# Performance work log

Hardware: AMD Instinct MI355X
Metric: run time of the kernel (lower is better)

## Reference

```python
import jax, jax.numpy as jnp
import numpy as np

# static 3D multi-scale configuration (transoar-style)
SS = np.array([[24, 24, 24], [12, 12, 12], [6, 6, 6], [3, 3, 3]], dtype=np.int64)  # (D,H,W) per level
NPL = SS.prod(1)
LSI = np.concatenate([[0], np.cumsum(NPL)[:-1]]).astype(np.int64)
S = int(NPL.sum())  # 15795 flattened tokens
B, C, HH, L, P = 2, 256, 8, 4, 4
DH = C // HH
NQ, FF = 80, 1024
NENC, NDEC = 6, 6
EPS = 1e-5


def layer_norm(x, g, b):
    mu = jnp.mean(x, -1, keepdims=True)
    var = jnp.mean((x - mu) ** 2, -1, keepdims=True)
    return (x - mu) * jax.lax.rsqrt(var + EPS) * g + b


def mha(q, k, v, in_w, in_b, out_w, out_b, mask=None):
    # torch nn.MultiheadAttention math (batch-first layout here)
    wq, wk, wv = jnp.split(in_w, 3, 0)
    bq, bk, bv = jnp.split(in_b, 3, 0)
    qh = (q @ wq.T + bq).reshape(B, -1, HH, DH)
    kh = (k @ wk.T + bk).reshape(B, -1, HH, DH)
    vh = (v @ wv.T + bv).reshape(B, -1, HH, DH)
    logits = jnp.einsum('bqhd,bkhd->bhqk', qh, kh) / jnp.float32(np.sqrt(DH))
    if mask is not None:  # bool mask, True = blocked
        logits = jnp.where(mask[None, None], jnp.float32(-1e9), logits)
    att = jax.nn.softmax(logits, -1)
    o = jnp.einsum('bhqk,bkhd->bqhd', att, vh).reshape(B, -1, C)
    return o @ out_w.T + out_b


def ms_deform_attn(query, ref, value_in, off_w, off_b, aw_w, aw_b, val_w, val_b, out_w, out_b):
    # 3D multi-scale deformable attention (deformable-DETR, trilinear sampling,
    # zero padding outside, align_corners=False semantics)
    Nq = query.shape[1]
    value = (value_in @ val_w.T + val_b).reshape(B, S, HH, DH)
    off = (query @ off_w.T + off_b).reshape(B, Nq, HH, L, P, 3)
    aw = jax.nn.softmax((query @ aw_w.T + aw_b).reshape(B, Nq, HH, L * P), -1)
    aw = aw.reshape(B, Nq, HH, L, P)
    norm = jnp.asarray(SS[:, ::-1].copy(), jnp.float32)  # (W,H,D) per level -> xyz order
    loc = ref[:, :, None, :, None, :] + off / norm[None, None, None, :, None, :]  # [B,Nq,HH,L,P,3]
    out = jnp.zeros((B, Nq, HH, DH), query.dtype)
    for lvl in range(L):
        D_, H_, W_ = (int(s) for s in SS[lvl])
        s0 = int(LSI[lvl])
        v = value[:, s0:s0 + D_ * H_ * W_].transpose(0, 2, 1, 3).reshape(B * HH, D_ * H_ * W_, DH)
        l = loc[:, :, :, lvl].transpose(0, 2, 1, 3, 4).reshape(B * HH, Nq * P, 3)
        x = l[..., 0] * W_ - 0.5
        y = l[..., 1] * H_ - 0.5
        z = l[..., 2] * D_ - 0.5
        x0, y0, z0 = jnp.floor(x), jnp.floor(y), jnp.floor(z)
        samp = jnp.zeros((B * HH, Nq * P, DH), query.dtype)
        for dz in (0, 1):
            for dy in (0, 1):
                for dx in (0, 1):
                    xi, yi, zi = x0 + dx, y0 + dy, z0 + dz
                    w = (1 - jnp.abs(x - xi)) * (1 - jnp.abs(y - yi)) * (1 - jnp.abs(z - zi))
                    ok = (xi >= 0) & (xi < W_) & (yi >= 0) & (yi < H_) & (zi >= 0) & (zi < D_)
                    idx = ((jnp.clip(zi, 0, D_ - 1) * H_ + jnp.clip(yi, 0, H_ - 1)) * W_
                           + jnp.clip(xi, 0, W_ - 1)).astype(jnp.int32)
                    samp = samp + jnp.take_along_axis(v, idx[..., None], axis=1) * (w * ok)[..., None]
        samp = samp.reshape(B, HH, Nq, P, DH)
        out = out + jnp.einsum('bhqpd,bhqp->bqhd', samp, aw[:, :, :, lvl].transpose(0, 2, 1, 3))
    return out.reshape(B, Nq, C) @ out_w.T + out_b


def get_reference_points(valid_ratios):
    refs = []
    for D_, H_, W_ in SS:
        z = (np.arange(D_) + 0.5) / D_
        y = (np.arange(H_) + 0.5) / H_
        x = (np.arange(W_) + 0.5) / W_
        zz, yy, xx = np.meshgrid(z, y, x, indexing='ij')
        refs.append(np.stack([xx.ravel(), yy.ravel(), zz.ravel()], -1))
    ref = jnp.asarray(np.concatenate(refs, 0).astype(np.float32))  # [S,3] xyz
    return ref[None, :, None, :] * valid_ratios[:, None]  # [B,S,L,3]


def _forward(fl, attn_mask):
    (src, pos, lvl_pos, tgt, query_pos, valid_ratios,
     eow, eob, eaw, eab, evw, evb, eouw, eoub, el1g, el1b, ef1w, ef1b, ef2w, ef2b, el2g, el2b,
     dsiw, dsib, dsow, dsob, dciw, dcib, dcow, dcob,
     dl1g, dl1b, dl2g, dl2b, dl3g, dl3b, df1w, df1b, df2w, df2b) = fl
    ref = get_reference_points(valid_ratios)
    out = src
    for i in range(NENC):
        a = ms_deform_attn(out + pos, ref, out, eow[i], eob[i], eaw[i], eab[i],
                           evw[i], evb[i], eouw[i], eoub[i])
        out = layer_norm(out + a, el1g[i], el1b[i])
        h = jax.nn.relu(out @ ef1w[i].T + ef1b[i])
        out = layer_norm(out + h @ ef2w[i].T + ef2b[i], el2g[i], el2b[i])
    memory = out
    q = tgt
    for i in range(NDEC):
        qk = q + query_pos
        sa = mha(qk, qk, q, dsiw[i], dsib[i], dsow[i], dsob[i])
        q = layer_norm(q + sa, dl2g[i], dl2b[i])
        ca = mha(q + query_pos, memory + lvl_pos, memory, dciw[i], dcib[i], dcow[i], dcob[i],
                 mask=attn_mask)
        q = layer_norm(q + ca, dl1g[i], dl1b[i])
        h = jax.nn.relu(q @ df1w[i].T + df1b[i])
        q = layer_norm(q + h @ df2w[i].T + df2b[i], dl3g[i], dl3b[i])
    return q


def setup_inputs() -> dict:
    key = jax.random.key(0)
    it = iter(jax.random.split(key, 64))
    def nrm(shape, s=0.02):
        return jax.random.normal(next(it), shape, jnp.float32) * s
    HLPO, HLP = HH * L * P * 3, HH * L * P
    inp = {}
    inp['src'] = nrm((B, S, C), 1.0)
    inp['pos'] = nrm((B, S, C), 1.0)
    inp['lvl_pos'] = nrm((B, S, C), 1.0)
    inp['tgt'] = nrm((B, NQ, C), 1.0)
    inp['query_pos'] = nrm((B, NQ, C), 1.0)
    inp['valid_ratios'] = jnp.ones((B, L, 3), jnp.float32)
    inp['enc_off_w'] = nrm((NENC, HLPO, C))
    inp['enc_off_b'] = nrm((NENC, HLPO), 0.1)
    inp['enc_aw_w'] = nrm((NENC, HLP, C))
    inp['enc_aw_b'] = jnp.zeros((NENC, HLP), jnp.float32)
    inp['enc_val_w'] = nrm((NENC, C, C))
    inp['enc_val_b'] = jnp.zeros((NENC, C), jnp.float32)
    inp['enc_out_w'] = nrm((NENC, C, C))
    inp['enc_out_b'] = jnp.zeros((NENC, C), jnp.float32)
    inp['enc_ln1_g'] = jnp.ones((NENC, C), jnp.float32)
    inp['enc_ln1_b'] = jnp.zeros((NENC, C), jnp.float32)
    inp['enc_fc1_w'] = nrm((NENC, FF, C))
    inp['enc_fc1_b'] = jnp.zeros((NENC, FF), jnp.float32)
    inp['enc_fc2_w'] = nrm((NENC, C, FF))
    inp['enc_fc2_b'] = jnp.zeros((NENC, C), jnp.float32)
    inp['enc_ln2_g'] = jnp.ones((NENC, C), jnp.float32)
    inp['enc_ln2_b'] = jnp.zeros((NENC, C), jnp.float32)
    inp['dec_sa_in_w'] = nrm((NDEC, 3 * C, C))
    inp['dec_sa_in_b'] = jnp.zeros((NDEC, 3 * C), jnp.float32)
    inp['dec_sa_out_w'] = nrm((NDEC, C, C))
    inp['dec_sa_out_b'] = jnp.zeros((NDEC, C), jnp.float32)
    inp['dec_ca_in_w'] = nrm((NDEC, 3 * C, C))
    inp['dec_ca_in_b'] = jnp.zeros((NDEC, 3 * C), jnp.float32)
    inp['dec_ca_out_w'] = nrm((NDEC, C, C))
    inp['dec_ca_out_b'] = jnp.zeros((NDEC, C), jnp.float32)
    inp['dec_ln1_g'] = jnp.ones((NDEC, C), jnp.float32)
    inp['dec_ln1_b'] = jnp.zeros((NDEC, C), jnp.float32)
    inp['dec_ln2_g'] = jnp.ones((NDEC, C), jnp.float32)
    inp['dec_ln2_b'] = jnp.zeros((NDEC, C), jnp.float32)
    inp['dec_ln3_g'] = jnp.ones((NDEC, C), jnp.float32)
    inp['dec_ln3_b'] = jnp.zeros((NDEC, C), jnp.float32)
    inp['dec_fc1_w'] = nrm((NDEC, FF, C))
    inp['dec_fc1_b'] = jnp.zeros((NDEC, FF), jnp.float32)
    inp['dec_fc2_w'] = nrm((NDEC, C, FF))
    inp['dec_fc2_b'] = jnp.zeros((NDEC, C), jnp.float32)
    inp['attn_mask'] = jax.random.bernoulli(next(it), 0.5, (NQ, S))
    inp['spatial_shapes'] = jnp.asarray(SS, jnp.int32)
    inp['level_start_index'] = jnp.asarray(LSI, jnp.int32)
    return inp


def reference(src, pos, lvl_pos, tgt, query_pos, valid_ratios,
              enc_off_w, enc_off_b, enc_aw_w, enc_aw_b, enc_val_w, enc_val_b, enc_out_w, enc_out_b,
              enc_ln1_g, enc_ln1_b, enc_fc1_w, enc_fc1_b, enc_fc2_w, enc_fc2_b, enc_ln2_g, enc_ln2_b,
              dec_sa_in_w, dec_sa_in_b, dec_sa_out_w, dec_sa_out_b,
              dec_ca_in_w, dec_ca_in_b, dec_ca_out_w, dec_ca_out_b,
              dec_ln1_g, dec_ln1_b, dec_ln2_g, dec_ln2_b, dec_ln3_g, dec_ln3_b,
              dec_fc1_w, dec_fc1_b, dec_fc2_w, dec_fc2_b,
              attn_mask, spatial_shapes, level_start_index):
    fl = (src, pos, lvl_pos, tgt, query_pos, valid_ratios,
          enc_off_w, enc_off_b, enc_aw_w, enc_aw_b, enc_val_w, enc_val_b, enc_out_w, enc_out_b,
          enc_ln1_g, enc_ln1_b, enc_fc1_w, enc_fc1_b, enc_fc2_w, enc_fc2_b, enc_ln2_g, enc_ln2_b,
          dec_sa_in_w, dec_sa_in_b, dec_sa_out_w, dec_sa_out_b,
          dec_ca_in_w, dec_ca_in_b, dec_ca_out_w, dec_ca_out_b,
          dec_ln1_g, dec_ln1_b, dec_ln2_g, dec_ln2_b, dec_ln3_g, dec_ln3_b,
          dec_fc1_w, dec_fc1_b, dec_fc2_w, dec_fc2_b)
    return _forward(fl, attn_mask)
```

## Files before the change

kernel.cpp:

```cpp
#include <hip/hip_runtime.h>
#include <cstdint>

#define S_TOT 15795
#define B_SZ 2
#define NQ 80
#define XSPLIT 128
#define NSPLIT 124
#define XCHUNK 128
#define MP 31616

typedef __attribute__((ext_vector_type(8))) short short8;
typedef __attribute__((ext_vector_type(4))) float f32x4;

__device__ __forceinline__ unsigned short f2bf(float f) {
    unsigned u = __float_as_uint(f);
    unsigned r = u + 0x7fffu + ((u >> 16) & 1u);
    return (unsigned short)(r >> 16);
}

__global__ __launch_bounds__(256)
void cast_bf16_kernel(const float* __restrict__ x, unsigned short* __restrict__ o, int n4)
{
    int i = blockIdx.x * 256 + threadIdx.x;
    if (i < n4) {
        float4 v = ((const float4*)x)[i];
        ushort4 r;
        r.x = f2bf(v.x); r.y = f2bf(v.y); r.z = f2bf(v.z); r.w = f2bf(v.w);
        ((ushort4*)o)[i] = r;
    }
}

__global__ __launch_bounds__(256)
void cast_fuse_w_kernel(const float* __restrict__ eow, const float* __restrict__ eaw,
                        unsigned short* __restrict__ o)
{
    int i = blockIdx.x * 256 + threadIdx.x;
    const int n4 = 6 * 512 * 256 / 4;
    if (i < n4) {
        int e = i * 4;
        int layer = e / (512 * 256);
        int rem = e - layer * 512 * 256;
        int row = rem >> 8, col = rem & 255;
        const float* src = (row < 384)
            ? eow + ((size_t)layer * 384 + row) * 256 + col
            : eaw + ((size_t)layer * 128 + (row - 384)) * 256 + col;
        float4 v = *(const float4*)src;
        ushort4 r;
        r.x = f2bf(v.x); r.y = f2bf(v.y); r.z = f2bf(v.z); r.w = f2bf(v.w);
        ((ushort4*)o)[i] = r;
    }
}

__global__ __launch_bounds__(512)
void fuse_bias_kernel(const float* __restrict__ eob, const float* __restrict__ eab,
                      float* __restrict__ o)
{
    int i = blockIdx.x, t = threadIdx.x;
    o[i * 512 + t] = (t < 384) ? eob[i * 384 + t] : eab[i * 128 + (t - 384)];
}

__global__ __launch_bounds__(256)
void mask_pack_kernel(const unsigned char* __restrict__ mask,
                      unsigned long long* __restrict__ mp, int Lk)
{
    __shared__ unsigned char ml[80][260];
    const int k0 = blockIdx.x * 256;
    const int t = threadIdx.x;
    for (int idx = t; idx < 80 * 256; idx += 256) {
        int q = idx >> 8, kk = idx & 255;
        int kg = k0 + kk;
        ml[q][kk] = (kg < Lk) ? mask[(size_t)q * Lk + kg] : 1;
    }
    __syncthreads();
    int kg = k0 + t;
    if (kg < Lk) {
        unsigned long long lo = 0, hi = 0;
        #pragma unroll
        for (int q = 0; q < 64; ++q)
            lo |= (unsigned long long)(ml[q][t] ? 1u : 0u) << q;
        #pragma unroll
        for (int q = 0; q < 16; ++q)
            hi |= (unsigned long long)(ml[64 + q][t] ? 1u : 0u) << q;
        mp[2 * kg] = lo; mp[2 * kg + 1] = hi;
    }
}

__global__ __launch_bounds__(256)
void add_bf16_kernel(const float* __restrict__ a, const float* __restrict__ b,
                     unsigned short* __restrict__ o, int n4)
{
    int i = blockIdx.x * 256 + threadIdx.x;
    if (i < n4) {
        float4 av = ((const float4*)a)[i];
        float4 bv = ((const float4*)b)[i];
        ushort4 r;
        r.x = f2bf(av.x + bv.x); r.y = f2bf(av.y + bv.y);
        r.z = f2bf(av.z + bv.z); r.w = f2bf(av.w + bv.w);
        ((ushort4*)o)[i] = r;
    }
}

__global__ __launch_bounds__(256)
void gemm_bf16_kernel(const unsigned short* __restrict__ A,
                      const unsigned short* __restrict__ B,
                      const float* __restrict__ bias, void* __restrict__ Yv,
                      int M, int N, int K, int mode)
{
    __shared__ unsigned short As[2][128 * 32];
    __shared__ unsigned short Bs[2][128 * 32];
    const int t = threadIdx.x;
    const int wave = t >> 6, lane = t & 63;
    const int quad = lane >> 4, l16 = lane & 15;
    const int bm0 = blockIdx.y * 128;
    const int bn0 = blockIdx.x * 128;
    const int wm = (wave & 1) * 64;
    const int wn = (wave >> 1) * 64;
    const int srow = t >> 2;
    const int scol = (t & 3) * 8;

    f32x4 acc[4][4] = {};

    const unsigned short* pa0 = A + (size_t)(bm0 + srow) * K + scol;
    const unsigned short* pa1 = pa0 + (size_t)64 * K;
    const unsigned short* pb0 = B + (size_t)(bn0 + srow) * K + scol;
    const unsigned short* pb1 = pb0 + (size_t)64 * K;

    const int nk = K / 32;
    short8 a0 = *(const short8*)(pa0);
    short8 a1 = *(const short8*)(pa1);
    short8 b0 = *(const short8*)(pb0);
    short8 b1 = *(const short8*)(pb1);
    *(short8*)&As[0][srow * 32 + scol] = a0;
    *(short8*)&As[0][(srow + 64) * 32 + scol] = a1;
    *(short8*)&Bs[0][srow * 32 + scol] = b0;
    *(short8*)&Bs[0][(srow + 64) * 32 + scol] = b1;
    __syncthreads();

    for (int kb = 0; kb < nk; ++kb) {
        const int cur = kb & 1, nxt = cur ^ 1;
        const bool more = (kb + 1) < nk;
        if (more) {
            const int k0 = (kb + 1) * 32;
            a0 = *(const short8*)(pa0 + k0);
            a1 = *(const short8*)(pa1 + k0);
            b0 = *(const short8*)(pb0 + k0);
            b1 = *(const short8*)(pb1 + k0);
        }

        short8 af[4], bf[4];
        #pragma unroll
        for (int im = 0; im < 4; ++im)
            af[im] = *(const short8*)&As[cur][(wm + im * 16 + l16) * 32 + quad * 8];
        #pragma unroll
        for (int in = 0; in < 4; ++in)
            bf[in] = *(const short8*)&Bs[cur][(wn + in * 16 + l16) * 32 + quad * 8];
        #pragma unroll
        for (int im = 0; im < 4; ++im)
            #pragma unroll
            for (int in = 0; in < 4; ++in)
                acc[im][in] = __builtin_amdgcn_mfma_f32_16x16x32_bf16(
                    af[im], bf[in], acc[im][in], 0, 0, 0);

        if (more) {
            *(short8*)&As[nxt][srow * 32 + scol] = a0;
            *(short8*)&As[nxt][(srow + 64) * 32 + scol] = a1;
            *(short8*)&Bs[nxt][srow * 32 + scol] = b0;
            *(short8*)&Bs[nxt][(srow + 64) * 32 + scol] = b1;
        }
        __syncthreads();
    }

    #pragma unroll
    for (int im = 0; im < 4; ++im) {
        const int gm0 = bm0 + wm + im * 16 + quad * 4;
        #pragma unroll
        for (int in = 0; in < 4; ++in) {
            const int gn = bn0 + wn + in * 16 + l16;
            const float bv = bias[gn];
            #pragma unroll
            for (int r = 0; r < 4; ++r) {
                int row = gm0 + r;
                if (row < M) {
                    float o = acc[im][in][r] + bv;
                    if (mode == 0) {
                        ((float*)Yv)[(size_t)row * N + gn] = o;
                    } else {
                        if (mode == 1) o = fmaxf(o, 0.f);
                        ((unsigned short*)Yv)[(size_t)row * N + gn] = f2bf(o);
                    }
                }
            }
        }
    }
}

__global__ __launch_bounds__(256)
void gemm_bias_kernel(const float* __restrict__ X, const float* __restrict__ Xadd,
                      const float* __restrict__ W,
                      const float* __restrict__ bias, float* __restrict__ Y,
                      int M, int N, int K, int relu)
{
    __shared__ float Xs[16][68];
    __shared__ float Ws[16][68];
    const int bm0 = blockIdx.y * 64;
    const int bn0 = blockIdx.x * 64;
    const int t = threadIdx.x;
    const int tx = t & 15, ty = t >> 4;
    const int lr = t >> 2;
    const int lk = (t & 3) << 2;
    float acc[4][4] = {};
    const int xr = bm0 + lr;
    const int wr = bn0 + lr;
    const float* xp = X + (size_t)xr * K + lk;
    const float* xap = Xadd ? Xadd + (size_t)xr * K + lk : nullptr;
    const float* wp = W + (size_t)wr * K + lk;
    for (int k0 = 0; k0 < K; k0 += 16) {
        float4 xv = make_float4(0.f, 0.f, 0.f, 0.f);
        if (xr < M) {
            xv = *(const float4*)(xp + k0);
            if (xap) {
                float4 av = *(const float4*)(xap + k0);
                xv.x += av.x; xv.y += av.y; xv.z += av.z; xv.w += av.w;
            }
        }
        float4 wv = make_float4(0.f, 0.f, 0.f, 0.f);
        if (wr < N) wv = *(const float4*)(wp + k0);
        Xs[lk + 0][lr] = xv.x; Xs[lk + 1][lr] = xv.y;
        Xs[lk + 2][lr] = xv.z; Xs[lk + 3][lr] = xv.w;
        Ws[lk + 0][lr] = wv.x; Ws[lk + 1][lr] = wv.y;
        Ws[lk + 2][lr] = wv.z; Ws[lk + 3][lr] = wv.w;
        __syncthreads();
        #pragma unroll
        for (int k = 0; k < 16; ++k) {
            float a0 = Xs[k][ty * 4 + 0], a1 = Xs[k][ty * 4 + 1];
            float a2 = Xs[k][ty * 4 + 2], a3 = Xs[k][ty * 4 + 3];
            float b0 = Ws[k][tx * 4 + 0], b1 = Ws[k][tx * 4 + 1];
            float b2 = Ws[k][tx * 4 + 2], b3 = Ws[k][tx * 4 + 3];
            acc[0][0] += a0 * b0; acc[0][1] += a0 * b1; acc[0][2] += a0 * b2; acc[0][3] += a0 * b3;
            acc[1][0] += a1 * b0; acc[1][1] += a1 * b1; acc[1][2] += a1 * b2; acc[1][3] += a1 * b3;
            acc[2][0] += a2 * b0; acc[2][1] += a2 * b1; acc[2][2] += a2 * b2; acc[2][3] += a2 * b3;
            acc[3][0] += a3 * b0; acc[3][1] += a3 * b1; acc[3][2] += a3 * b2; acc[3][3] += a3 * b3;
        }
        __syncthreads();
    }
    const int c0 = bn0 + tx * 4;
    float4 bv = *(const float4*)(bias + c0);
    #pragma unroll
    for (int i = 0; i < 4; ++i) {
        int r = bm0 + ty * 4 + i;
        if (r >= M) continue;
        float4 o;
        o.x = acc[i][0] + bv.x; o.y = acc[i][1] + bv.y;
        o.z = acc[i][2] + bv.z; o.w = acc[i][3] + bv.w;
        if (relu) {
            o.x = fmaxf(o.x, 0.f); o.y = fmaxf(o.y, 0.f);
            o.z = fmaxf(o.z, 0.f); o.w = fmaxf(o.w, 0.f);
        }
        *(float4*)(Y + (size_t)r * N + c0) = o;
    }
}

__global__ __launch_bounds__(256)
void ln_res_kernel(const float* __restrict__ X, const float* __restrict__ R,
                   const float* __restrict__ g, const float* __restrict__ bta,
                   float* __restrict__ O, unsigned short* __restrict__ Ob,
                   const float* __restrict__ Padd, unsigned short* __restrict__ Oadd,
                   int nrows)
{
    const int row = blockIdx.x * 4 + (threadIdx.x >> 6);
    if (row >= nrows) return;
    const int t = threadIdx.x & 63;
    const float* x = X + (size_t)row * 256;
    const float* r = R + (size_t)row * 256;
    float v[4];
    float s = 0.f;
    #pragma unroll
    for (int i = 0; i < 4; ++i) { int c = t + 64 * i; v[i] = x[c] + r[c]; s += v[i]; }
    #pragma unroll
    for (int off = 32; off >= 1; off >>= 1) s += __shfl_xor(s, off, 64);
    float mu = s * (1.f / 256.f);
    float s2 = 0.f;
    #pragma unroll
    for (int i = 0; i < 4; ++i) { float d = v[i] - mu; s2 += d * d; }
    #pragma unroll
    for (int off = 32; off >= 1; off >>= 1) s2 += __shfl_xor(s2, off, 64);
    float rstd = rsqrtf(s2 * (1.f / 256.f) + 1e-5f);
    #pragma unroll
    for (int i = 0; i < 4; ++i) {
        int c = t + 64 * i;
        float o = (v[i] - mu) * rstd * g[c] + bta[c];
        O[(size_t)row * 256 + c] = o;
        if (Ob) Ob[(size_t)row * 256 + c] = f2bf(o);
        if (Oadd) Oadd[(size_t)row * 256 + c] = f2bf(o + Padd[(size_t)row * 256 + c]);
    }
}

__global__ __launch_bounds__(256)
void deform_kernel(const float* __restrict__ offaw,
                   const unsigned short* __restrict__ value,
                   unsigned short* __restrict__ out)
{
    const int nwg = B_SZ * S_TOT;
    const int qq = nwg >> 3, rr = nwg & 7;
    const int xcd = blockIdx.x & 7, chunk_off = blockIdx.x >> 3;
    const int bq = (xcd < rr ? xcd * (qq + 1) : rr * (qq + 1) + (xcd - rr) * qq) + chunk_off;
    const int b = bq / S_TOT;
    const int s = bq - b * S_TOT;
    const int t = threadIdx.x;

    __shared__ float2 tbl[128][8];

    if (t < 128) {
        const int h = t >> 4, lp = t & 15, l = lp >> 2;
        float logit = offaw[(size_t)bq * 512 + 384 + t];
        float m = logit;
        m = fmaxf(m, __shfl_xor(m, 1, 64));
        m = fmaxf(m, __shfl_xor(m, 2, 64));
        m = fmaxf(m, __shfl_xor(m, 4, 64));
        m = fmaxf(m, __shfl_xor(m, 8, 64));
        float e = __expf(logit - m);
        float su = e;
        su += __shfl_xor(su, 1, 64);
        su += __shfl_xor(su, 2, 64);
        su += __shfl_xor(su, 4, 64);
        su += __shfl_xor(su, 8, 64);
        float aw = e / su;

        int nq_, sq0;
        if (s < 13824)      { nq_ = 24; sq0 = 0; }
        else if (s < 15552) { nq_ = 12; sq0 = 13824; }
        else if (s < 15768) { nq_ = 6;  sq0 = 15552; }
        else                { nq_ = 3;  sq0 = 15768; }
        int tl = s - sq0;
        int iz = tl / (nq_ * nq_);
        int r1 = tl - iz * nq_ * nq_;
        int iy = r1 / nq_;
        int ix = r1 - iy * nq_;
        float invn = 1.f / (float)nq_;
        float rx = (ix + 0.5f) * invn;
        float ry = (iy + 0.5f) * invn;
        float rz = (iz + 0.5f) * invn;

        const int lvl_n[4]  = {24, 12, 6, 3};
        const int lvl_s0[4] = {0, 13824, 15552, 15768};
        const int nl = lvl_n[l];
        const int s0l = lvl_s0[l];
        const float* op = offaw + (size_t)bq * 512 + t * 3;
        float x = rx * nl + op[0] - 0.5f;
        float y = ry * nl + op[1] - 0.5f;
        float z = rz * nl + op[2] - 0.5f;
        float fx = floorf(x), fy = floorf(y), fz = floorf(z);
        int x0 = (int)fx, y0 = (int)fy, z0 = (int)fz;
        float wx1 = x - fx, wx0 = 1.f - wx1;
        float wy1 = y - fy, wy0 = 1.f - wy1;
        float wz1 = z - fz, wz0 = 1.f - wz1;
        int xc0 = min(max(x0, 0), nl - 1), xc1 = min(max(x0 + 1, 0), nl - 1);
        int yc0 = min(max(y0, 0), nl - 1), yc1 = min(max(y0 + 1, 0), nl - 1);
        int zc0 = min(max(z0, 0), nl - 1), zc1 = min(max(z0 + 1, 0), nl - 1);
        bool ox0 = (x0 >= 0) && (x0 < nl);
        bool ox1 = (x0 + 1 >= 0) && (x0 + 1 < nl);
        bool oy0 = (y0 >= 0) && (y0 < nl), oy1 = (y0 + 1 >= 0) && (y0 + 1 < nl);
        bool oz0 = (z0 >= 0) && (z0 < nl), oz1 = (z0 + 1 >= 0) && (z0 + 1 < nl);
        int base = b * S_TOT + s0l;
        #pragma unroll
        for (int c = 0; c < 8; ++c) {
            int dx = c & 1, dy = (c >> 1) & 1, dz = c >> 2;
            float w = (dx ? wx1 : wx0) * (dy ? wy1 : wy0) * (dz ? wz1 : wz0);
            bool ok = (dx ? ox1 : ox0) && (dy ? oy1 : oy0) && (dz ? oz1 : oz0);
            int xi = dx ? xc1 : xc0;
            int yi = dy ? yc1 : yc0;
            int zi = dz ? zc1 : zc0;
            int elem = ((base + (zi * nl + yi) * nl + xi) * 8 + h) * 32;
            tbl[t][c] = make_float2(ok ? w * aw : 0.f, __int_as_float(elem));
        }
    }
    __syncthreads();

    const int c16 = t & 3, z = t >> 2, cr = z & 7, h = z >> 3;
    const float2* trow = &tbl[h * 16][cr];
    float acc[8] = {0.f, 0.f, 0.f, 0.f, 0.f, 0.f, 0.f, 0.f};
    #pragma unroll
    for (int p = 0; p < 16; ++p) {
        float2 e = trow[p * 8];
        const uint4 dv = *(const uint4*)(value + (size_t)__float_as_int(e.y) + c16 * 8);
        float w = e.x;
        acc[0] += w * __uint_as_float(dv.x << 16);
        acc[1] += w * __uint_as_float(dv.x & 0xffff0000u);
        acc[2] += w * __uint_as_float(dv.y << 16);
        acc[3] += w * __uint_as_float(dv.y & 0xffff0000u);
        acc[4] += w * __uint_as_float(dv.z << 16);
        acc[5] += w * __uint_as_float(dv.z & 0xffff0000u);
        acc[6] += w * __uint_as_float(dv.w << 16);
        acc[7] += w * __uint_as_float(dv.w & 0xffff0000u);
    }
    #pragma unroll
    for (int i = 0; i < 8; ++i) {
        acc[i] += __shfl_xor(acc[i], 4, 64);
        acc[i] += __shfl_xor(acc[i], 8, 64);
        acc[i] += __shfl_xor(acc[i], 16, 64);
    }
    if ((t & 28) == 0) {
        uint4 r;
        r.x = (unsigned)f2bf(acc[0]) | ((unsigned)f2bf(acc[1]) << 16);
        r.y = (unsigned)f2bf(acc[2]) | ((unsigned)f2bf(acc[3]) << 16);
        r.z = (unsigned)f2bf(acc[4]) | ((unsigned)f2bf(acc[5]) << 16);
        r.w = (unsigned)f2bf(acc[6]) | ((unsigned)f2bf(acc[7]) << 16);
        *(uint4*)(out + (size_t)bq * 256 + h * 32 + c16 * 8) = r;
    }
}

__global__ __launch_bounds__(256)
void attn_kernel(const float* __restrict__ Q, const float* __restrict__ K,
                 const float* __restrict__ V, float* __restrict__ O,
                 int Lq, int Lk, float scale, int ldq, int ldk)
{
    const int nqc = (Lq + 3) >> 2;
    const int blk = blockIdx.x;
    const int qc = blk % nqc;
    const int bh = blk / nqc;
    const int h = bh & 7;
    const int b = bh >> 3;
    const int qi0 = qc * 4;
    const int t = threadIdx.x;
    const int c = t & 31, g = t >> 5;

    float qv[4];
    #pragma unroll
    for (int j = 0; j < 4; ++j)
        qv[j] = Q[((size_t)(b * Lq + qi0 + j)) * ldq + h * 32 + c];

    float m[4], l[4], acc[4];
    #pragma unroll
    for (int j = 0; j < 4; ++j) { m[j] = -1e30f; l[j] = 0.f; acc[j] = 0.f; }

    for (int k = g; k < Lk; k += 8) {
        float kv = K[((size_t)(b * Lk + k)) * ldk + h * 32 + c];
        float vv = V[((size_t)(b * Lk + k)) * 256 + h * 32 + c];
        #pragma unroll
        for (int j = 0; j < 4; ++j) {
            float p = qv[j] * kv;
            p += __shfl_xor(p, 16, 32);
            p += __shfl_xor(p, 8, 32);
            p += __shfl_xor(p, 4, 32);
            p += __shfl_xor(p, 2, 32);
            p += __shfl_xor(p, 1, 32);
            float sc = p * scale;
            float mn = fmaxf(m[j], sc);
            float fo = __expf(m[j] - mn);
            float w = __expf(sc - mn);
            l[j] = l[j] * fo + w;
            acc[j] = acc[j] * fo + w * vv;
            m[j] = mn;
        }
    }
    __shared__ float sm[8][4], sl[8][4], sacc[8][4][32];
    if (c == 0) {
        #pragma unroll
        for (int j = 0; j < 4; ++j) { sm[g][j] = m[j]; sl[g][j] = l[j]; }
    }
    #pragma unroll
    for (int j = 0; j < 4; ++j) sacc[g][j][c] = acc[j];
    __syncthreads();
    if (g == 0) {
        #pragma unroll
        for (int j = 0; j < 4; ++j) {
            float M = -1e30f;
            #pragma unroll
            for (int i = 0; i < 8; ++i) M = fmaxf(M, sm[i][j]);
            float L = 0.f, o = 0.f;
            #pragma unroll
            for (int i = 0; i < 8; ++i) {
                float e = __expf(sm[i][j] - M);
                L += sl[i][j] * e;
                o += sacc[i][j][c] * e;
            }
            O[((size_t)(b * Lq + qi0 + j)) * 256 + h * 32 + c] = o / L;
        }
    }
}

__global__ __launch_bounds__(320)
void xattn_part_kernel(const float* __restrict__ Q,
                       const unsigned short* __restrict__ K,
                       const unsigned short* __restrict__ V,
                       const unsigned long long* __restrict__ mp,
                       float* __restrict__ pm, float* __restrict__ pl,
                       float* __restrict__ po, int Lk, float scale)
{
    const int split = blockIdx.x;
    const int bh = blockIdx.y;
    const int b = bh >> 3, h = bh & 7;
    const int t = threadIdx.x;
    const int wave = t >> 6, lane = t & 63;
    const int l16 = lane & 15, quad = lane >> 4;

    __shared__ unsigned short Ks[128][40];
    __shared__ unsigned short Vt[32][136];
    __shared__ unsigned short Ps[80][40];
    __shared__ unsigned long long Mw[2][128];

    const int k_base = split * XCHUNK;

    for (int idx = t; idx < 512; idx += 320) {
        int key = idx >> 2, cg = (idx & 3) * 8;
        int kg = k_base + key;
        short8 kv = {0, 0, 0, 0, 0, 0, 0, 0};
        short8 vv = {0, 0, 0, 0, 0, 0, 0, 0};
        if (kg < Lk) {
            size_t go = ((size_t)(b * Lk + kg)) * 256 + h * 32 + cg;
            kv = *(const short8*)(K + go);
            vv = *(const short8*)(V + go);
        }
        *(short8*)&Ks[key][cg] = kv;
        #pragma unroll
        for (int j = 0; j < 8; ++j)
            Vt[cg + j][key] = (unsigned short)vv[j];
    }
    if (t < 128) {
        int kg = k_base + t;
        unsigned long long lo = ~0ULL, hi = ~0ULL;
        if (kg < Lk) { lo = mp[2 * kg]; hi = mp[2 * kg + 1]; }
        Mw[0][t] = lo; Mw[1][t] = hi;
    }

    const int q = wave * 16 + l16;
    short8 qf;
    {
        const float* qp = Q + ((size_t)(b * NQ + q)) * 256 + h * 32 + quad * 8;
        float4 q0 = *(const float4*)qp;
        float4 q1 = *(const float4*)(qp + 4);
        unsigned short* qh = (unsigned short*)&qf;
        qh[0] = f2bf(q0.x * scale); qh[1] = f2bf(q0.y * scale);
        qh[2] = f2bf(q0.z * scale); qh[3] = f2bf(q0.w * scale);
        qh[4] = f2bf(q1.x * scale); qh[5] = f2bf(q1.y * scale);
        qh[6] = f2bf(q1.z * scale); qh[7] = f2bf(q1.w * scale);
    }
    __syncthreads();

    f32x4 sfr[8];
    const f32x4 zz = {0.f, 0.f, 0.f, 0.f};
    #pragma unroll
    for (int tt = 0; tt < 8; ++tt) {
        short8 kf = *(const short8*)&Ks[tt * 16 + l16][quad * 8];
        sfr[tt] = __builtin_amdgcn_mfma_f32_16x16x32_bf16(kf, qf, zz, 0, 0, 0);
    }

    const unsigned long long* mrow = Mw[wave >> 2];
    const int qbit = (wave < 4 ? wave * 16 : 0) + l16;
    const int widx = qbit >> 5;
    const int sh = qbit & 31;

    float sc[8][4];
    #pragma unroll
    for (int tt = 0; tt < 8; ++tt) {
        int k0 = tt * 16 + quad * 4;
        uint4 ma = *(const uint4*)&mrow[k0];
        uint4 mb = *(const uint4*)&mrow[k0 + 2];
        unsigned w0 = widx ? ma.y : ma.x;
        unsigned w1 = widx ? ma.w : ma.z;
        unsigned w2 = widx ? mb.y : mb.x;
        unsigned w3 = widx ? mb.w : mb.z;
        sc[tt][0] = ((w0 >> sh) & 1u) ? -1e9f : sfr[tt][0];
        sc[tt][1] = ((w1 >> sh) & 1u) ? -1e9f : sfr[tt][1];
        sc[tt][2] = ((w2 >> sh) & 1u) ? -1e9f : sfr[tt][2];
        sc[tt][3] = ((w3 >> sh) & 1u) ? -1e9f : sfr[tt][3];
    }
    float mx = -1e30f;
    #pragma unroll
    for (int tt = 0; tt < 8; ++tt)
        #pragma unroll
        for (int r = 0; r < 4; ++r) mx = fmaxf(mx, sc[tt][r]);
    mx = fmaxf(mx, __shfl_xor(mx, 16, 64));
    mx = fmaxf(mx, __shfl_xor(mx, 32, 64));
    float sum = 0.f;
    #pragma unroll
    for (int tt = 0; tt < 8; ++tt)
        #pragma unroll
        for (int r = 0; r < 4; ++r) {
            sc[tt][r] = __expf(sc[tt][r] - mx);
            sum += sc[tt][r];
        }
    sum += __shfl_xor(sum, 16, 64);
    sum += __shfl_xor(sum, 32, 64);

    f32x4 oacc[2] = {zz, zz};
    #pragma unroll
    for (int s = 0; s < 4; ++s) {
        #pragma unroll
        for (int tt = 0; tt < 2; ++tt) {
            int T = s * 2 + tt;
            unsigned plo = (unsigned)f2bf(sc[T][0]) | ((unsigned)f2bf(sc[T][1]) << 16);
            unsigned phi = (unsigned)f2bf(sc[T][2]) | ((unsigned)f2bf(sc[T][3]) << 16);
            unsigned* dst = (unsigned*)&Ps[q][tt * 16 + quad * 4];
            dst[0] = plo; dst[1] = phi;
        }
        asm volatile("" ::: "memory");
        short8 pf = *(const short8*)&Ps[q][quad * 8];
        short8 vf0 = *(const short8*)&Vt[l16][s * 32 + quad * 8];
        short8 vf1 = *(const short8*)&Vt[16 + l16][s * 32 + quad * 8];
        oacc[0] = __builtin_amdgcn_mfma_f32_16x16x32_bf16(vf0, pf, oacc[0], 0, 0, 0);
        oacc[1] = __builtin_amdgcn_mfma_f32_16x16x32_bf16(vf1, pf, oacc[1], 0, 0, 0);
    }

    const size_t obase = ((size_t)bh * NSPLIT + split) * NQ;
    #pragma unroll
    for (int c = 0; c < 2; ++c)
        #pragma unroll
        for (int r = 0; r < 4; ++r)
            po[(obase + q) * 32 + c * 16 + quad * 4 + r] = oacc[c][r];
    if (quad == 0) { pm[obase + q] = mx; pl[obase + q] = sum; }
}

__global__ __launch_bounds__(64)
void xattn_merge_kernel(const float* __restrict__ pm, const float* __restrict__ pl,
                        const float* __restrict__ po, float* __restrict__ O)
{
    const int idx = blockIdx.x;
    const int bh = idx / NQ, q = idx - bh * NQ;
    const int b = bh >> 3, h = bh & 7;
    const int tt = threadIdx.x;
    if (tt >= 32) return;
    const int c = tt;
    float M = -1e30f;
    for (int s = 0; s < NSPLIT; ++s)
        M = fmaxf(M, pm[((size_t)bh * NSPLIT + s) * NQ + q]);
    float L = 0.f, o = 0.f;
    for (int s = 0; s < NSPLIT; ++s) {
        size_t base = ((size_t)bh * NSPLIT + s) * NQ + q;
        float e = __expf(pm[base] - M);
        L += pl[base] * e;
        o += po[base * 32 + c] * e;
    }
    O[((size_t)(b * NQ + q)) * 256 + h * 32 + c] = o / L;
}

extern "C" void kernel_launch(void* const* d_in, const int* in_sizes, int n_in,
                              void* d_out, int out_size, void* d_ws, size_t ws_size,
                              hipStream_t stream)
{
    const float* src       = (const float*)d_in[0];
    const float* pos       = (const float*)d_in[1];
    const float* lvl_pos   = (const float*)d_in[2];
    const float* tgt       = (const float*)d_in[3];
    const float* query_pos = (const float*)d_in[4];
    const float* eow  = (const float*)d_in[6];
    const float* eob  = (const float*)d_in[7];
    const float* eaw  = (const float*)d_in[8];
    const float* eab  = (const float*)d_in[9];
    const float* evw  = (const float*)d_in[10];
    const float* evb  = (const float*)d_in[11];
    const float* eouw = (const float*)d_in[12];
    const float* eoub = (const float*)d_in[13];
    const float* el1g = (const float*)d_in[14];
    const float* el1b = (const float*)d_in[15];
    const float* ef1w = (const float*)d_in[16];
    const float* ef1b = (const float*)d_in[17];
    const float* ef2w = (const float*)d_in[18];
    const float* ef2b = (const float*)d_in[19];
    const float* el2g = (const float*)d_in[20];
    const float* el2b = (const float*)d_in[21];
    const float* dsiw = (const float*)d_in[22];
    const float* dsib = (const float*)d_in[23];
    const float* dsow = (const float*)d_in[24];
    const float* dsob = (const float*)d_in[25];
    const float* dciw = (const float*)d_in[26];
    const float* dcib = (const float*)d_in[27];
    const float* dcow = (const float*)d_in[28];
    const float* dcob = (const float*)d_in[29];
    const float* dl1g = (const float*)d_in[30];
    const float* dl1b = (const float*)d_in[31];
    const float* dl2g = (const float*)d_in[32];
    const float* dl2b = (const float*)d_in[33];
    const float* dl3g = (const float*)d_in[34];
    const float* dl3b = (const float*)d_in[35];
    const float* df1w = (const float*)d_in[36];
    const float* df1b = (const float*)d_in[37];
    const float* df2w = (const float*)d_in[38];
    const float* df2b = (const float*)d_in[39];
    const unsigned char* amask = (const unsigned char*)d_in[40];

    const int MBS = B_SZ * S_TOT;
    const size_t nBSC = (size_t)MBS * 256;
    const size_t nP   = (size_t)MP * 256;
    const size_t nFFA = (size_t)MBS * 512 + 16384;

    float* ws = (float*)d_ws;
    float* f_out = ws; ws += nP;
    float* f_mlp = ws; ws += nP;
    float* f_ffa = ws; ws += nFFA;
    float* f_offaw = f_ffa;
    float* f_val = ws; ws += nP;
    float* d_q   = ws; ws += 40960;
    float* d_qkp = ws; ws += 81920;
    float* d_sq  = ws; ws += 40960;
    float* d_sv  = ws; ws += 40960;
    float* d_ao  = ws; ws += 40960;
    float* d_pr  = ws; ws += 40960;
    float* d_h   = ws; ws += 163840;
    float* x_pm  = ws; ws += (size_t)16 * XSPLIT * NQ;
    float* x_pl  = ws; ws += (size_t)16 * XSPLIT * NQ;
    float* x_po  = ws; ws += (size_t)16 * XSPLIT * NQ * 32;
    unsigned long long* x_mp = (unsigned long long*)ws; ws += 2 * 16384;
    float* f_fb  = ws; ws += 6 * 512;

    unsigned short* bws = (unsigned short*)ws;
    unsigned short* b_mlp  = bws; bws += nP;
    unsigned short* b_out  = bws; bws += nP;
    unsigned short* w_eoaw = bws; bws += (size_t)6 * 512 * 256;
    unsigned short* w_evw  = bws; bws += (size_t)6 * 256 * 256;
    unsigned short* w_eouw = bws; bws += (size_t)6 * 256 * 256;
    unsigned short* w_ef1  = bws; bws += (size_t)6 * 1024 * 256;
    unsigned short* w_ef2  = bws; bws += (size_t)6 * 256 * 1024;
    unsigned short* w_dciw = bws; bws += (size_t)6 * 768 * 256;

    unsigned short* b_hs   = (unsigned short*)f_ffa;
    unsigned short* b_samp = b_mlp;
    unsigned short* b_val  = (unsigned short*)x_pm;
    unsigned short* b_xk   = (unsigned short*)f_offaw;
    unsigned short* b_xv   = (unsigned short*)f_val;

    auto gemmb = [&](const unsigned short* A, const unsigned short* W, const float* bb,
                     void* Y, int M, int N, int K, int mode) {
        dim3 grid(N / 128, (M + 127) / 128);
        gemm_bf16_kernel<<<grid, dim3(256), 0, stream>>>(A, W, bb, Y, M, N, K, mode);
    };
    auto gemms = [&](const float* X, const float* Xadd, const float* W, const float* bb,
                     float* Y, int M, int N, int K, int relu) {
        dim3 grid(N / 64, (M + 63) / 64);
        gemm_bias_kernel<<<grid, dim3(256), 0, stream>>>(X, Xadd, W, bb, Y, M, N, K, relu);
    };
    auto cast = [&](const float* x, unsigned short* o, size_t n) {
        int n4c = (int)(n / 4);
        cast_bf16_kernel<<<(n4c + 255) / 256, 256, 0, stream>>>(x, o, n4c);
    };

    const int n4 = (int)(nBSC / 4);
    const float scale = 0.17677669529663687f;
    const int lnGrid = (MBS + 3) / 4;

    {
        const int nf4 = 6 * 512 * 256 / 4;
        cast_fuse_w_kernel<<<(nf4 + 255) / 256, 256, 0, stream>>>(eow, eaw, w_eoaw);
        fuse_bias_kernel<<<6, 512, 0, stream>>>(eob, eab, f_fb);
        mask_pack_kernel<<<(S_TOT + 255) / 256, 256, 0, stream>>>(amask, x_mp, S_TOT);
    }
    cast(evw,  w_evw,  (size_t)6 * 256 * 256);
    cast(eouw, w_eouw, (size_t)6 * 256 * 256);
    cast(ef1w, w_ef1,  (size_t)6 * 1024 * 256);
    cast(ef2w, w_ef2,  (size_t)6 * 256 * 1024);
    cast(dciw, w_dciw, (size_t)6 * 768 * 256);

    hipMemcpyAsync(f_out, src, nBSC * sizeof(float), hipMemcpyDeviceToDevice, stream);
    cast(src, b_out, nBSC);
    add_bf16_kernel<<<(n4 + 255) / 256, 256, 0, stream>>>(f_out, pos, b_mlp, n4);

    for (int i = 0; i < 6; ++i) {
        gemmb(b_mlp, w_eoaw + (size_t)i * 512 * 256, f_fb + i * 512, f_offaw, MBS, 512, 256, 0);
        gemmb(b_out, w_evw + (size_t)i * 256 * 256, evb + i * 256, b_val, MBS, 256, 256, 2);
        deform_kernel<<<MBS, 256, 0, stream>>>(f_offaw, b_val, b_samp);
        gemmb(b_samp, w_eouw + (size_t)i * 256 * 256, eoub + i * 256, f_mlp, MBS, 256, 256, 0);
        ln_res_kernel<<<lnGrid, 256, 0, stream>>>(f_out, f_mlp, el1g + i * 256, el1b + i * 256,
                                                  f_out, b_out, (const float*)nullptr,
                                                  (unsigned short*)nullptr, MBS);
        gemmb(b_out, w_ef1 + (size_t)i * 1024 * 256, ef1b + i * 1024, b_hs, MBS, 1024, 256, 1);
        gemmb(b_hs, w_ef2 + (size_t)i * 256 * 1024, ef2b + i * 256, f_val, MBS, 256, 1024, 0);
        ln_res_kernel<<<lnGrid, 256, 0, stream>>>(f_out, f_val, el2g + i * 256, el2b + i * 256,
                                                  f_out, b_out, (i < 5 ? pos : lvl_pos),
                                                  b_mlp, MBS);
    }

    hipMemcpyAsync(d_q, tgt, 40960 * sizeof(float), hipMemcpyDeviceToDevice, stream);

    for (int i = 0; i < 6; ++i) {
        const float* siw = dsiw + (size_t)i * 768 * 256;
        const float* sib = dsib + (size_t)i * 768;
        gemms(d_q, query_pos, siw, sib, d_qkp, 160, 512, 256, 0);
        gemms(d_q, nullptr, siw + 512 * 256, sib + 512, d_sv, 160, 256, 256, 0);
        attn_kernel<<<B_SZ * 8 * (NQ / 4), 256, 0, stream>>>(
            d_qkp, d_qkp + 256, d_sv, d_ao, NQ, NQ, scale, 512, 512);
        gemms(d_ao, nullptr, dsow + (size_t)i * 256 * 256, dsob + i * 256, d_pr, 160, 256, 256, 0);
        ln_res_kernel<<<40, 256, 0, stream>>>(d_q, d_pr, dl2g + i * 256, dl2b + i * 256,
                                              d_q, (unsigned short*)nullptr,
                                              (const float*)nullptr, (unsigned short*)nullptr, 160);

        const float* cib = dcib + (size_t)i * 768;
        gemms(d_q, query_pos, dciw + (size_t)i * 768 * 256, cib, d_sq, 160, 256, 256, 0);
        gemmb(b_mlp, w_dciw + (size_t)i * 768 * 256 + 256 * 256, cib + 256,
              b_xk, MBS, 256, 256, 2);
        gemmb(b_out, w_dciw + (size_t)i * 768 * 256 + 512 * 256, cib + 512,
              b_xv, MBS, 256, 256, 2);
        xattn_part_kernel<<<dim3(NSPLIT, 16), 320, 0, stream>>>(
            d_sq, b_xk, b_xv, x_mp, x_pm, x_pl, x_po, S_TOT, scale);
        xattn_merge_kernel<<<16 * NQ, 64, 0, stream>>>(x_pm, x_pl, x_po, d_ao);
        gemms(d_ao, nullptr, dcow + (size_t)i * 256 * 256, dcob + i * 256, d_pr, 160, 256, 256, 0);
        ln_res_kernel<<<40, 256, 0, stream>>>(d_q, d_pr, dl1g + i * 256, dl1b + i * 256,
                                              d_q, (unsigned short*)nullptr,
                                              (const float*)nullptr, (unsigned short*)nullptr, 160);

        gemms(d_q, nullptr, df1w + (size_t)i * 1024 * 256, df1b + i * 1024, d_h, 160, 1024, 256, 1);
        gemms(d_h, nullptr, df2w + (size_t)i * 256 * 1024, df2b + i * 256, d_pr, 160, 256, 1024, 0);
        ln_res_kernel<<<40, 256, 0, stream>>>(d_q, d_pr, dl3g + i * 256, dl3b + i * 256,
                                              d_q, (unsigned short*)nullptr,
                                              (const float*)nullptr, (unsigned short*)nullptr, 160);
    }

    hipMemcpyAsync(d_out, d_q, 40960 * sizeof(float), hipMemcpyDeviceToDevice, stream);
}
```

Baseline: 4.080 ms.

## Use direct global-to-LDS loads in GEMM, pad deform table, specialize index math

The GEMM main loop now stages A/B tiles with global_load_lds builtins that write straight into shared memory, in place of loading into registers and then storing to LDS. This saves VGPRs and the separate store instructions, and lets the prefetch for the next tile overlap the MFMA work. In the deformable-attention kernel the sampling table gets a padded row stride of 9 to reduce LDS bank conflicts. The per-level index arithmetic is also rewritten to divide by compile-time constants. The LDS layout of the direct loads must match the per-lane layout the old code produced (wave*512 offsets versus srow*32+scol), so correctness relies on the lane-to-address mapping lining up.

```diff
diff --git a/kernel.cpp b/kernel.cpp
--- a/kernel.cpp
+++ b/kernel.cpp
@@ -125,26 +125,27 @@
     const unsigned short* pb0 = B + (size_t)(bn0 + srow) * K + scol;
     const unsigned short* pb1 = pb0 + (size_t)64 * K;
 
+    #define GLL(src, dst)                                                        \
+        __builtin_amdgcn_global_load_lds(                                        \
+            (const __attribute__((address_space(1))) unsigned int*)(const void*)(src), \
+            (__attribute__((address_space(3))) unsigned int*)(void*)(dst),       \
+            16, 0, 0)
+
     const int nk = K / 32;
-    short8 a0 = *(const short8*)(pa0);
-    short8 a1 = *(const short8*)(pa1);
-    short8 b0 = *(const short8*)(pb0);
-    short8 b1 = *(const short8*)(pb1);
-    *(short8*)&As[0][srow * 32 + scol] = a0;
-    *(short8*)&As[0][(srow + 64) * 32 + scol] = a1;
-    *(short8*)&Bs[0][srow * 32 + scol] = b0;
-    *(short8*)&Bs[0][(srow + 64) * 32 + scol] = b1;
+    GLL(pa0, &As[0][wave * 512]);
+    GLL(pa1, &As[0][2048 + wave * 512]);
+    GLL(pb0, &Bs[0][wave * 512]);
+    GLL(pb1, &Bs[0][2048 + wave * 512]);
     __syncthreads();
 
     for (int kb = 0; kb < nk; ++kb) {
         const int cur = kb & 1, nxt = cur ^ 1;
-        const bool more = (kb + 1) < nk;
-        if (more) {
+        if (kb + 1 < nk) {
             const int k0 = (kb + 1) * 32;
-            a0 = *(const short8*)(pa0 + k0);
-            a1 = *(const short8*)(pa1 + k0);
-            b0 = *(const short8*)(pb0 + k0);
-            b1 = *(const short8*)(pb1 + k0);
+            GLL(pa0 + k0, &As[nxt][wave * 512]);
+            GLL(pa1 + k0, &As[nxt][2048 + wave * 512]);
+            GLL(pb0 + k0, &Bs[nxt][wave * 512]);
+            GLL(pb1 + k0, &Bs[nxt][2048 + wave * 512]);
         }
 
         short8 af[4], bf[4];
@@ -161,14 +162,9 @@
                 acc[im][in] = __builtin_amdgcn_mfma_f32_16x16x32_bf16(
                     af[im], bf[in], acc[im][in], 0, 0, 0);
 
-        if (more) {
-            *(short8*)&As[nxt][srow * 32 + scol] = a0;
-            *(short8*)&As[nxt][(srow + 64) * 32 + scol] = a1;
-            *(short8*)&Bs[nxt][srow * 32 + scol] = b0;
-            *(short8*)&Bs[nxt][(srow + 64) * 32 + scol] = b1;
-        }
         __syncthreads();
     }
+    #undef GLL
 
     #pragma unroll
     for (int im = 0; im < 4; ++im) {
@@ -308,7 +304,7 @@
     const int s = bq - b * S_TOT;
     const int t = threadIdx.x;
 
-    __shared__ float2 tbl[128][8];
+    __shared__ float2 tbl[128][9];
 
     if (t < 128) {
         const int h = t >> 4, lp = t & 15, l = lp >> 2;
@@ -326,17 +322,19 @@
         su += __shfl_xor(su, 8, 64);
         float aw = e / su;
 
-        int nq_, sq0;
-        if (s < 13824)      { nq_ = 24; sq0 = 0; }
-        else if (s < 15552) { nq_ = 12; sq0 = 13824; }
-        else if (s < 15768) { nq_ = 6;  sq0 = 15552; }
-        else                { nq_ = 3;  sq0 = 15768; }
-        int tl = s - sq0;
-        int iz = tl / (nq_ * nq_);
-        int r1 = tl - iz * nq_ * nq_;
-        int iy = r1 / nq_;
-        int ix = r1 - iy * nq_;
-        float invn = 1.f / (float)nq_;
+        int nq_, iz, iy, ix; float invn;
+        if (s < 13824)      { nq_ = 24; invn = 1.f / 24.f; int tl = s;
+                              iz = tl / 576; int r1 = tl - iz * 576;
+                              iy = r1 / 24;  ix = r1 - iy * 24; }
+        else if (s < 15552) { nq_ = 12; invn = 1.f / 12.f; int tl = s - 13824;
+                              iz = tl / 144; int r1 = tl - iz * 144;
+                              iy = r1 / 12;  ix = r1 - iy * 12; }
+        else if (s < 15768) { nq_ = 6;  invn = 1.f / 6.f;  int tl = s - 15552;
+                              iz = tl / 36;  int r1 = tl - iz * 36;
+                              iy = r1 / 6;   ix = r1 - iy * 6; }
+        else                { nq_ = 3;  invn = 1.f / 3.f;  int tl = s - 15768;
+                              iz = tl / 9;   int r1 = tl - iz * 9;
+                              iy = r1 / 3;   ix = r1 - iy * 3; }
         float rx = (ix + 0.5f) * invn;
         float ry = (iy + 0.5f) * invn;
         float rz = (iz + 0.5f) * invn;
@@ -381,7 +379,7 @@
     float acc[8] = {0.f, 0.f, 0.f, 0.f, 0.f, 0.f, 0.f, 0.f};
     #pragma unroll
     for (int p = 0; p < 16; ++p) {
-        float2 e = trow[p * 8];
+        float2 e = trow[p * 9];
         const uint4 dv = *(const uint4*)(value + (size_t)__float_as_int(e.y) + c16 * 8);
         float w = e.x;
         acc[0] += w * __uint_as_float(dv.x << 16);
```

New measurement: 4.060 ms. Within noise of the previous version (-0.5%).
